# Kernel tuning notes

Hardware: AMD Instinct MI355X
Metric: run time of the kernel (lower is better)

The kernel has to match this reference:

```python
import jax, jax.numpy as jnp
import numpy as np

HID, NH, NKV, HD = 2048, 16, 8, 128
EPS = 1e-6
THETA = 10000.0
SCALE = HD ** -0.5


def setup_inputs() -> dict:
    key = jax.random.key(0)
    ks = jax.random.split(key, 6)
    S = 2048
    return {
        "positions": jnp.arange(S, dtype=jnp.int32),
        "hidden_states": jax.random.normal(ks[0], (S, HID), dtype=jnp.float32),
        "layernorm_weight": jax.random.uniform(ks[1], (HID,), dtype=jnp.float32, minval=0.5, maxval=1.5),
        "w_qkv": jax.random.normal(ks[2], ((NH + 2 * NKV) * HD, HID), dtype=jnp.float32) * 0.02,
        "w_o": jax.random.normal(ks[3], (HID, NH * HD), dtype=jnp.float32) * 0.02,
        "q_norm_w": jax.random.uniform(ks[4], (HD,), dtype=jnp.float32, minval=0.5, maxval=1.5),
        "k_norm_w": jax.random.uniform(ks[5], (HD,), dtype=jnp.float32, minval=0.5, maxval=1.5),
    }


def _rmsnorm(x, w, eps=EPS):
    var = jnp.mean(jnp.square(x), axis=-1, keepdims=True)
    return x * jax.lax.rsqrt(var + eps) * w


def _rope(x, cos, sin):
    # x: [S, h, HD]; cos/sin: [S, 1, HD//2] (neox-style rotate-half)
    x1, x2 = x[..., : HD // 2], x[..., HD // 2 :]
    return jnp.concatenate([x1 * cos - x2 * sin, x2 * cos + x1 * sin], axis=-1)


def reference(positions, hidden_states, layernorm_weight, w_qkv, w_o, q_norm_w, k_norm_w):
    S = hidden_states.shape[0]
    # Fused RMSNorm + QKV projection
    hn = _rmsnorm(hidden_states, layernorm_weight)
    qkv = hn @ w_qkv.T  # [S, (NH+2*NKV)*HD]
    q, k, v = jnp.split(qkv, [NH * HD, (NH + NKV) * HD], axis=-1)
    q = q.reshape(S, NH, HD)
    k = k.reshape(S, NKV, HD)
    v = v.reshape(S, NKV, HD)
    # Per-head QK RMSNorm
    q = _rmsnorm(q, q_norm_w)
    k = _rmsnorm(k, k_norm_w)
    # RoPE
    inv_freq = 1.0 / (THETA ** (jnp.arange(0, HD, 2, dtype=jnp.float32) / HD))
    freqs = positions.astype(jnp.float32)[:, None] * inv_freq  # [S, HD//2]
    cos = jnp.cos(freqs)[:, None, :]
    sin = jnp.sin(freqs)[:, None, :]
    q = _rope(q, cos, sin)
    k = _rope(k, cos, sin)
    # GQA: expand kv heads to match query heads
    rep = NH // NKV
    k = jnp.repeat(k, rep, axis=1)  # [S, NH, HD]
    v = jnp.repeat(v, rep, axis=1)
    # Causal attention
    scores = jnp.einsum("shd,thd->hst", q, k) * SCALE  # [NH, S, S]
    causal = jnp.tril(jnp.ones((S, S), dtype=bool))
    scores = jnp.where(causal, scores, jnp.finfo(scores.dtype).min)
    probs = jax.nn.softmax(scores, axis=-1)
    out = jnp.einsum("hst,thd->shd", probs, v)  # [S, NH, HD]
    # Output projection
    return out.reshape(S, NH * HD) @ w_o.T
```

## Files before the change

### kernel.cpp

```cpp
#include <hip/hip_runtime.h>
#include <hip/hip_bf16.h>
#include <math.h>

#define HID 2048
#define NH 16
#define NKV 8
#define HD 128
#define SEQ 2048
#define EPS 1e-6f
#define SCALE 0.08838834764831845f

typedef __attribute__((ext_vector_type(8))) short bf8_t;
typedef __attribute__((ext_vector_type(4))) float f4_t;

__device__ __forceinline__ short f2bf(float f) {
    union { __hip_bfloat16 h; short s; } u;
    u.h = __float2bfloat16(f);
    return u.s;
}
__device__ __forceinline__ float bf2f(short s) {
    union { short s; __hip_bfloat16 h; } u;
    u.s = s;
    return __bfloat162float(u.h);
}
__device__ __forceinline__ bf8_t pack8(const float4& a, const float4& b) {
    bf8_t r;
    r[0] = f2bf(a.x); r[1] = f2bf(a.y); r[2] = f2bf(a.z); r[3] = f2bf(a.w);
    r[4] = f2bf(b.x); r[5] = f2bf(b.y); r[6] = f2bf(b.z); r[7] = f2bf(b.w);
    return r;
}
__device__ __forceinline__ void gload16(const short* g, short* l) {
    __builtin_amdgcn_global_load_lds(
        (const __attribute__((address_space(1))) unsigned int*)g,
        (__attribute__((address_space(3))) unsigned int*)l, 16, 0, 0);
}

__device__ __forceinline__ float wave_reduce_sum(float v) {
#pragma unroll
    for (int off = 32; off > 0; off >>= 1) v += __shfl_xor(v, off);
    return v;
}

__global__ __launch_bounds__(256) void f2bf_kernel(
    const float* __restrict__ src, short* __restrict__ dst, int n8) {
    int i = blockIdx.x * 256 + threadIdx.x;
    if (i < n8) {
        float4 a = *(const float4*)(src + (size_t)i * 8);
        float4 b = *(const float4*)(src + (size_t)i * 8 + 4);
        *(bf8_t*)(dst + (size_t)i * 8) = pack8(a, b);
    }
}

__global__ __launch_bounds__(256) void rmsnorm_hid_kernel(
    const float* __restrict__ x, const float* __restrict__ w,
    short* __restrict__ out) {
    int row = blockIdx.x;
    int tid = threadIdx.x;
    const float* xr = x + (size_t)row * HID;
    float4 a = *(const float4*)(xr + tid * 8);
    float4 b = *(const float4*)(xr + tid * 8 + 4);
    float ss = a.x * a.x + a.y * a.y + a.z * a.z + a.w * a.w +
               b.x * b.x + b.y * b.y + b.z * b.z + b.w * b.w;
    ss = wave_reduce_sum(ss);
    __shared__ float part[4];
    __shared__ float s_scale;
    if ((tid & 63) == 0) part[tid >> 6] = ss;
    __syncthreads();
    if (tid == 0) {
        float t = part[0] + part[1] + part[2] + part[3];
        s_scale = rsqrtf(t / (float)HID + EPS);
    }
    __syncthreads();
    float sc = s_scale;
    float4 wa = *(const float4*)(w + tid * 8);
    float4 wb = *(const float4*)(w + tid * 8 + 4);
    float4 oa = make_float4(a.x * sc * wa.x, a.y * sc * wa.y,
                            a.z * sc * wa.z, a.w * sc * wa.w);
    float4 ob = make_float4(b.x * sc * wb.x, b.y * sc * wb.y,
                            b.z * sc * wb.z, b.w * sc * wb.w);
    *(bf8_t*)(out + (size_t)row * HID + tid * 8) = pack8(oa, ob);
}

template <int MODE>
__global__ __launch_bounds__(256) void gemm_mfma_kernel(
    const short* __restrict__ A, const short* __restrict__ B,
    float* __restrict__ Cf, short* __restrict__ Q, short* __restrict__ Kp,
    short* __restrict__ Vr, int M, int N, int K) {
    __shared__ short As[128][64];
    __shared__ short Bs[128][64];
    int tid = threadIdx.x;
    int wv = tid >> 6, lane = tid & 63;
    int n16 = lane & 15, qd = lane >> 4;
    int m0 = blockIdx.y * 128, n0 = blockIdx.x * 128;
    int wm = (wv >> 1) * 64, wn = (wv & 1) * 64;
    int sr8 = lane >> 3, slot = lane & 7;

    size_t ainv[4], binv[4];
#pragma unroll
    for (int it = 0; it < 4; ++it) {
        int row = wv * 32 + it * 8 + sr8;
        int chunk = (slot - row) & 7;
        ainv[it] = (size_t)(m0 + row) * K + chunk * 8;
        binv[it] = (size_t)(n0 + row) * K + chunk * 8;
    }

    f4_t acc[4][4];
#pragma unroll
    for (int i = 0; i < 4; ++i)
#pragma unroll
        for (int j = 0; j < 4; ++j) acc[i][j] = (f4_t){0.f, 0.f, 0.f, 0.f};

    for (int k0 = 0; k0 < K; k0 += 64) {
        __syncthreads();
#pragma unroll
        for (int it = 0; it < 4; ++it) {
            gload16(A + ainv[it] + k0, &As[wv * 32 + it * 8][0]);
            gload16(B + binv[it] + k0, &Bs[wv * 32 + it * 8][0]);
        }
        __syncthreads();

        bf8_t af[4][2], bf[4][2];
#pragma unroll
        for (int t = 0; t < 4; ++t)
#pragma unroll
            for (int ks = 0; ks < 2; ++ks) {
                int ar = wm + t * 16 + n16;
                af[t][ks] = *(const bf8_t*)&As[ar][(((ks * 4 + qd) + ar) & 7) * 8];
                int br = wn + t * 16 + n16;
                bf[t][ks] = *(const bf8_t*)&Bs[br][(((ks * 4 + qd) + br) & 7) * 8];
            }
#pragma unroll
        for (int ks = 0; ks < 2; ++ks)
#pragma unroll
            for (int mt = 0; mt < 4; ++mt)
#pragma unroll
                for (int nt = 0; nt < 4; ++nt)
                    acc[mt][nt] = __builtin_amdgcn_mfma_f32_16x16x32_bf16(
                        af[mt][ks], bf[nt][ks], acc[mt][nt], 0, 0, 0);
    }

#pragma unroll
    for (int mt = 0; mt < 4; ++mt)
#pragma unroll
        for (int nt = 0; nt < 4; ++nt)
#pragma unroll
            for (int r = 0; r < 4; ++r) {
                int gm = m0 + wm + mt * 16 + qd * 4 + r;
                int gn = n0 + wn + nt * 16 + n16;
                float v = acc[mt][nt][r];
                if (MODE == 0) {
                    Cf[(size_t)gm * N + gn] = v;
                } else {
                    if (gn < NH * HD)
                        Q[(size_t)gm * (NH * HD) + gn] = f2bf(v);
                    else if (gn < (NH + NKV) * HD)
                        Kp[(size_t)gm * (NKV * HD) + (gn - NH * HD)] = f2bf(v);
                    else
                        Vr[(size_t)gm * (NKV * HD) + (gn - (NH + NKV) * HD)] = f2bf(v);
                }
            }
}

__global__ __launch_bounds__(256) void transpose_v_kernel(
    const short* __restrict__ vr, short* __restrict__ vt) {
    __shared__ short t[64][64];
    int s0 = blockIdx.x * 64, d0 = blockIdx.y * 64;
    int tid = threadIdx.x;
    int sl = tid >> 3, ch = tid & 7;
#pragma unroll
    for (int it = 0; it < 2; ++it) {
        int s_local = it * 32 + sl;
        bf8_t vv = *(const bf8_t*)(vr + (size_t)(s0 + s_local) * (NKV * HD) + d0 + ch * 8);
        *(bf8_t*)&t[s_local][((ch + s_local) & 7) * 8] = vv;
    }
    __syncthreads();
#pragma unroll
    for (int it = 0; it < 2; ++it) {
        int d_local = it * 32 + sl;
        int sbase = ch * 8;
        bf8_t o;
#pragma unroll
        for (int j = 0; j < 8; ++j) {
            int s = sbase + j;
            o[j] = t[s][(((d_local >> 3) + s) & 7) * 8 + (d_local & 7)];
        }
        *(bf8_t*)(vt + (size_t)(d0 + d_local) * SEQ + s0 + sbase) = o;
    }
}

__global__ __launch_bounds__(128) void qknorm_rope_kernel(
    short* __restrict__ q, short* __restrict__ k,
    const float* __restrict__ qw, const float* __restrict__ kw,
    const int* __restrict__ pos) {
    int s = blockIdx.x;
    int hh = blockIdx.y;
    int d = threadIdx.x;
    short* ptr;
    const float* w;
    if (hh < NH) {
        ptr = q + (size_t)s * (NH * HD) + hh * HD;
        w = qw;
    } else {
        ptr = k + (size_t)s * (NKV * HD) + (hh - NH) * HD;
        w = kw;
    }
    float x = bf2f(ptr[d]);
    float ss = wave_reduce_sum(x * x);
    __shared__ float part[2];
    if ((d & 63) == 0) part[d >> 6] = ss;
    __syncthreads();
    float tot = part[0] + part[1];
    float xn = x * rsqrtf(tot / (float)HD + EPS) * w[d];
    __shared__ float sh[HD];
    sh[d] = xn;
    __syncthreads();
    int j = d & 63;
    float inv = powf(10000.0f, -(float)(2 * j) * (1.0f / (float)HD));
    float fr = (float)pos[s] * inv;
    float sn, cs;
    sincosf(fr, &sn, &cs);
    float o;
    if (d < 64)
        o = xn * cs - sh[d + 64] * sn;
    else
        o = xn * cs + sh[d - 64] * sn;
    ptr[d] = f2bf(o);
}

__device__ __forceinline__ void attn_stage(
    short (&kb)[64][128], short (&vb)[128][64],
    const short* __restrict__ kg, const short* __restrict__ vg,
    int t0, const int (&kinv)[4], const int (&vinv)[4], int wv) {
#pragma unroll
    for (int it = 0; it < 4; ++it) {
        gload16(kg + (size_t)t0 * (NKV * HD) + kinv[it], &kb[wv * 16 + it * 4][0]);
        gload16(vg + t0 + vinv[it], &vb[wv * 32 + it * 8][0]);
    }
}

__device__ __forceinline__ void attn_tile(
    const short (&kb)[64][128], const short (&vb)[128][64],
    short (&psh)[4][16][72],
    const bf8_t (&qf)[4], f4_t (&of)[8],
    float (&m_i)[4], float (&l_p)[4],
    int wv, int n, int qd, bool diag) {
    f4_t sc[4];
#pragma unroll
    for (int kk = 0; kk < 4; ++kk) sc[kk] = (f4_t){0.f, 0.f, 0.f, 0.f};
#pragma unroll
    for (int kk = 0; kk < 4; ++kk) {
        int key = kk * 16 + n;
#pragma unroll
        for (int ks = 0; ks < 4; ++ks) {
            bf8_t kf = *(const bf8_t*)&kb[key][(((ks * 4 + qd) + key) & 15) * 8];
            sc[kk] = __builtin_amdgcn_mfma_f32_16x16x32_bf16(qf[ks], kf, sc[kk], 0, 0, 0);
        }
    }
    int rowb = wv * 16 + qd * 4;
#pragma unroll
    for (int kk = 0; kk < 4; ++kk)
#pragma unroll
        for (int r = 0; r < 4; ++r) {
            float s = sc[kk][r] * SCALE;
            if (diag && (kk * 16 + n > rowb + r)) s = -1e30f;
            sc[kk][r] = s;
        }
#pragma unroll
    for (int r = 0; r < 4; ++r) {
        float mx = fmaxf(fmaxf(sc[0][r], sc[1][r]), fmaxf(sc[2][r], sc[3][r]));
#pragma unroll
        for (int off = 1; off < 16; off <<= 1) mx = fmaxf(mx, __shfl_xor(mx, off));
        float mnew = fmaxf(m_i[r], mx);
        float al = __expf(m_i[r] - mnew);
        m_i[r] = mnew;
        float lsum = 0.f;
#pragma unroll
        for (int kk = 0; kk < 4; ++kk) {
            float p = __expf(sc[kk][r] - mnew);
            psh[wv][qd * 4 + r][kk * 16 + n] = f2bf(p);
            lsum += p;
        }
        l_p[r] = l_p[r] * al + lsum;
#pragma unroll
        for (int nb = 0; nb < 8; ++nb) of[nb][r] *= al;
    }
    __builtin_amdgcn_wave_barrier();
#pragma unroll
    for (int ks2 = 0; ks2 < 2; ++ks2) {
        bf8_t pf = *(const bf8_t*)&psh[wv][n][ks2 * 32 + qd * 8];
#pragma unroll
        for (int nb = 0; nb < 8; ++nb) {
            int dim = nb * 16 + n;
            bf8_t vf = *(const bf8_t*)&vb[dim][(((ks2 * 4 + qd) + dim) & 7) * 8];
            of[nb] = __builtin_amdgcn_mfma_f32_16x16x32_bf16(pf, vf, of[nb], 0, 0, 0);
        }
    }
}

__global__ __launch_bounds__(256) void attn_mfma_kernel(
    const short* __restrict__ q, const short* __restrict__ k,
    const short* __restrict__ vt, short* __restrict__ o) {
    __shared__ short kbufA[64][128], kbufB[64][128];
    __shared__ short vbufA[128][64], vbufB[128][64];
    __shared__ short psh[4][16][72];

    int tid = threadIdx.x;
    int wv = tid >> 6, lane = tid & 63;
    int n = lane & 15, qd = lane >> 4;
    int bid = blockIdx.x;
    int p = bid & 255;
    int h, qb;
    if (bid < 256) { h = p >> 5;       qb = 31 - (p & 31); }
    else           { h = 8 + (p >> 5); qb = p & 31; }
    int kvh = h >> 1;
    int qbase = qb * 64;

    int kinv[4], vinv[4];
#pragma unroll
    for (int it = 0; it < 4; ++it) {
        int key = wv * 16 + it * 4 + (lane >> 4);
        int ck = ((lane & 15) - key) & 15;
        kinv[it] = key * (NKV * HD) + kvh * HD + ck * 8;
        int dim = wv * 32 + it * 8 + (lane >> 3);
        int cv = ((lane & 7) - dim) & 7;
        vinv[it] = (kvh * HD + dim) * SEQ + cv * 8;
    }

    bf8_t qf[4];
    {
        const short* qp = q + (size_t)(qbase + wv * 16 + n) * (NH * HD) + h * HD + qd * 8;
#pragma unroll
        for (int ks = 0; ks < 4; ++ks) qf[ks] = *(const bf8_t*)(qp + ks * 32);
    }

    f4_t of[8];
#pragma unroll
    for (int i = 0; i < 8; ++i) of[i] = (f4_t){0.f, 0.f, 0.f, 0.f};
    float m_i[4] = {-1e30f, -1e30f, -1e30f, -1e30f};
    float l_p[4] = {0.f, 0.f, 0.f, 0.f};

    int ntiles = qb + 1;
    attn_stage(kbufA, vbufA, k, vt, 0, kinv, vinv, wv);
    for (int tt = 0; tt < ntiles; tt += 2) {
        __syncthreads();
        if (tt + 1 < ntiles)
            attn_stage(kbufB, vbufB, k, vt, (tt + 1) * 64, kinv, vinv, wv);
        attn_tile(kbufA, vbufA, psh, qf, of, m_i, l_p, wv, n, qd, tt == qb);
        if (tt + 1 < ntiles) {
            __syncthreads();
            if (tt + 2 < ntiles)
                attn_stage(kbufA, vbufA, k, vt, (tt + 2) * 64, kinv, vinv, wv);
            attn_tile(kbufB, vbufB, psh, qf, of, m_i, l_p, wv, n, qd, tt + 1 == qb);
        }
    }

    float inv[4];
#pragma unroll
    for (int r = 0; r < 4; ++r) {
        float l = l_p[r];
#pragma unroll
        for (int off = 1; off < 16; off <<= 1) l += __shfl_xor(l, off);
        inv[r] = 1.0f / l;
    }
#pragma unroll
    for (int nb = 0; nb < 8; ++nb)
#pragma unroll
        for (int r = 0; r < 4; ++r) {
            int row = qbase + wv * 16 + qd * 4 + r;
            o[(size_t)row * (NH * HD) + h * HD + nb * 16 + n] = f2bf(of[nb][r] * inv[r]);
        }
}

extern "C" void kernel_launch(void* const* d_in, const int* in_sizes, int n_in,
                              void* d_out, int out_size, void* d_ws, size_t ws_size,
                              hipStream_t stream) {
    const int* positions   = (const int*)d_in[0];
    const float* hidden    = (const float*)d_in[1];
    const float* ln_w      = (const float*)d_in[2];
    const float* w_qkv     = (const float*)d_in[3];
    const float* w_o       = (const float*)d_in[4];
    const float* q_norm_w  = (const float*)d_in[5];
    const float* k_norm_w  = (const float*)d_in[6];
    float* out = (float*)d_out;

    char* base = (char*)d_ws;
    short* hnb  = (short*)(base);
    short* wqb  = (short*)(base + ((size_t)8 << 20));
    short* vtb  = (short*)(base + ((size_t)8 << 20));
    short* wob  = (short*)(base + ((size_t)24 << 20));
    short* qbf  = (short*)(base + ((size_t)32 << 20));
    short* kbf  = (short*)(base + ((size_t)40 << 20));
    short* vrow = (short*)(base + ((size_t)44 << 20));

    f2bf_kernel<<<4096, 256, 0, stream>>>(w_qkv, wqb, (NH + 2 * NKV) * HD * HID / 8);
    f2bf_kernel<<<2048, 256, 0, stream>>>(w_o, wob, HID * NH * HD / 8);
    rmsnorm_hid_kernel<<<SEQ, 256, 0, stream>>>(hidden, ln_w, hnb);
    gemm_mfma_kernel<1><<<dim3(32, 16), 256, 0, stream>>>(
        hnb, wqb, nullptr, qbf, kbf, vrow, SEQ, (NH + 2 * NKV) * HD, HID);
    transpose_v_kernel<<<dim3(SEQ / 64, NKV * HD / 64), 256, 0, stream>>>(vrow, vtb);
    qknorm_rope_kernel<<<dim3(SEQ, NH + NKV), 128, 0, stream>>>(
        qbf, kbf, q_norm_w, k_norm_w, positions);
    attn_mfma_kernel<<<512, 256, 0, stream>>>(qbf, kbf, vtb, hnb);
    gemm_mfma_kernel<0><<<dim3(16, 16), 256, 0, stream>>>(
        hnb, wob, out, nullptr, nullptr, nullptr, SEQ, NH * HD, HID);
}
```

Baseline: 293.0 us.

## Split long causal attention rows into KV chunks with merge; fuse small prep kernels

Attention for the upper 16 query blocks is split into two KV chunks, each computed by its own workgroup that writes unnormalised bf16 partials plus running max and sum. A new merge kernel combines the two chunks with log-sum-exp weights. This balances work across 768 workgroups instead of 512 uneven ones. The weight conversions and hidden-state RMSNorm are fused into one launch, as are the V transpose and QK-norm/RoPE, to cut launch count. The cost is an extra kernel, partial-result traffic, and bf16 rounding of the partials before the merge.

```diff
diff --git a/kernel.cpp b/kernel.cpp
--- a/kernel.cpp
+++ b/kernel.cpp
@@ -41,21 +41,28 @@
     return v;
 }
 
-__global__ __launch_bounds__(256) void f2bf_kernel(
-    const float* __restrict__ src, short* __restrict__ dst, int n8) {
-    int i = blockIdx.x * 256 + threadIdx.x;
-    if (i < n8) {
-        float4 a = *(const float4*)(src + (size_t)i * 8);
-        float4 b = *(const float4*)(src + (size_t)i * 8 + 4);
-        *(bf8_t*)(dst + (size_t)i * 8) = pack8(a, b);
-    }
-}
-
-__global__ __launch_bounds__(256) void rmsnorm_hid_kernel(
+__global__ __launch_bounds__(256) void prep_kernel(
+    const float* __restrict__ w_qkv, short* __restrict__ wqb,
+    const float* __restrict__ w_o, short* __restrict__ wob,
     const float* __restrict__ x, const float* __restrict__ w,
     short* __restrict__ out) {
-    int row = blockIdx.x;
+    int bid = blockIdx.x;
     int tid = threadIdx.x;
+    if (bid < 4096) {
+        int i = bid * 256 + tid;
+        float4 a = *(const float4*)(w_qkv + (size_t)i * 8);
+        float4 b = *(const float4*)(w_qkv + (size_t)i * 8 + 4);
+        *(bf8_t*)(wqb + (size_t)i * 8) = pack8(a, b);
+        return;
+    }
+    if (bid < 6144) {
+        int i = (bid - 4096) * 256 + tid;
+        float4 a = *(const float4*)(w_o + (size_t)i * 8);
+        float4 b = *(const float4*)(w_o + (size_t)i * 8 + 4);
+        *(bf8_t*)(wob + (size_t)i * 8) = pack8(a, b);
+        return;
+    }
+    int row = bid - 6144;
     const float* xr = x + (size_t)row * HID;
     float4 a = *(const float4*)(xr + tid * 8);
     float4 b = *(const float4*)(xr + tid * 8 + 4);
@@ -161,40 +168,41 @@
             }
 }
 
-__global__ __launch_bounds__(256) void transpose_v_kernel(
-    const short* __restrict__ vr, short* __restrict__ vt) {
-    __shared__ short t[64][64];
-    int s0 = blockIdx.x * 64, d0 = blockIdx.y * 64;
-    int tid = threadIdx.x;
-    int sl = tid >> 3, ch = tid & 7;
-#pragma unroll
-    for (int it = 0; it < 2; ++it) {
-        int s_local = it * 32 + sl;
-        bf8_t vv = *(const bf8_t*)(vr + (size_t)(s0 + s_local) * (NKV * HD) + d0 + ch * 8);
-        *(bf8_t*)&t[s_local][((ch + s_local) & 7) * 8] = vv;
-    }
-    __syncthreads();
-#pragma unroll
-    for (int it = 0; it < 2; ++it) {
-        int d_local = it * 32 + sl;
-        int sbase = ch * 8;
-        bf8_t o;
-#pragma unroll
-        for (int j = 0; j < 8; ++j) {
-            int s = sbase + j;
-            o[j] = t[s][(((d_local >> 3) + s) & 7) * 8 + (d_local & 7)];
-        }
-        *(bf8_t*)(vt + (size_t)(d0 + d_local) * SEQ + s0 + sbase) = o;
-    }
-}
-
-__global__ __launch_bounds__(128) void qknorm_rope_kernel(
+__global__ __launch_bounds__(256) void mid_kernel(
+    const short* __restrict__ vr, short* __restrict__ vt,
     short* __restrict__ q, short* __restrict__ k,
     const float* __restrict__ qw, const float* __restrict__ kw,
     const int* __restrict__ pos) {
-    int s = blockIdx.x;
-    int hh = blockIdx.y;
-    int d = threadIdx.x;
+    int bid = blockIdx.x;
+    int tid = threadIdx.x;
+    if (bid < 512) {
+        __shared__ short t[64][64];
+        int s0 = (bid & 31) * 64, d0 = (bid >> 5) * 64;
+        int sl = tid >> 3, ch = tid & 7;
+#pragma unroll
+        for (int it = 0; it < 2; ++it) {
+            int s_local = it * 32 + sl;
+            bf8_t vv = *(const bf8_t*)(vr + (size_t)(s0 + s_local) * (NKV * HD) + d0 + ch * 8);
+            *(bf8_t*)&t[s_local][((ch + s_local) & 7) * 8] = vv;
+        }
+        __syncthreads();
+#pragma unroll
+        for (int it = 0; it < 2; ++it) {
+            int d_local = it * 32 + sl;
+            int sbase = ch * 8;
+            bf8_t o;
+#pragma unroll
+            for (int j = 0; j < 8; ++j) {
+                int s = sbase + j;
+                o[j] = t[s][(((d_local >> 3) + s) & 7) * 8 + (d_local & 7)];
+            }
+            *(bf8_t*)(vt + (size_t)(d0 + d_local) * SEQ + s0 + sbase) = o;
+        }
+        return;
+    }
+    int u = (bid - 512) * 2 + (tid >> 7);
+    int ui = tid >> 7, d = tid & 127;
+    int s = u / 24, hh = u % 24;
     short* ptr;
     const float* w;
     if (hh < NH) {
@@ -206,13 +214,13 @@
     }
     float x = bf2f(ptr[d]);
     float ss = wave_reduce_sum(x * x);
-    __shared__ float part[2];
-    if ((d & 63) == 0) part[d >> 6] = ss;
+    __shared__ float part[2][2];
+    if ((d & 63) == 0) part[ui][d >> 6] = ss;
     __syncthreads();
-    float tot = part[0] + part[1];
+    float tot = part[ui][0] + part[ui][1];
     float xn = x * rsqrtf(tot / (float)HD + EPS) * w[d];
-    __shared__ float sh[HD];
-    sh[d] = xn;
+    __shared__ float sh[2][HD];
+    sh[ui][d] = xn;
     __syncthreads();
     int j = d & 63;
     float inv = powf(10000.0f, -(float)(2 * j) * (1.0f / (float)HD));
@@ -221,9 +229,9 @@
     sincosf(fr, &sn, &cs);
     float o;
     if (d < 64)
-        o = xn * cs - sh[d + 64] * sn;
+        o = xn * cs - sh[ui][d + 64] * sn;
     else
-        o = xn * cs + sh[d - 64] * sn;
+        o = xn * cs + sh[ui][d - 64] * sn;
     ptr[d] = f2bf(o);
 }
 
@@ -297,9 +305,10 @@
     }
 }
 
-__global__ __launch_bounds__(256) void attn_mfma_kernel(
+__global__ __launch_bounds__(256) void attn_chunk_kernel(
     const short* __restrict__ q, const short* __restrict__ k,
-    const short* __restrict__ vt, short* __restrict__ o) {
+    const short* __restrict__ vt, short* __restrict__ o,
+    short* __restrict__ opart, float* __restrict__ ml) {
     __shared__ short kbufA[64][128], kbufB[64][128];
     __shared__ short vbufA[128][64], vbufB[128][64];
     __shared__ short psh[4][16][72];
@@ -307,11 +316,26 @@
     int tid = threadIdx.x;
     int wv = tid >> 6, lane = tid & 63;
     int n = lane & 15, qd = lane >> 4;
+
     int bid = blockIdx.x;
-    int p = bid & 255;
-    int h, qb;
-    if (bid < 256) { h = p >> 5;       qb = 31 - (p & 31); }
-    else           { h = 8 + (p >> 5); qb = p & 31; }
+    int h, qb, tstart, tcount, c;
+    bool split;
+    if (bid < 512) {
+        int id = bid;
+        qb = 16 + (id >> 5);
+        c = (id >> 4) & 1;
+        h = id & 15;
+        if (c == 0) { tstart = 0; tcount = 16; }
+        else        { tstart = 16; tcount = qb - 15; }
+        split = true;
+    } else {
+        int id = bid - 512;
+        qb = 15 - (id >> 4);
+        h = id & 15;
+        tstart = 0; tcount = qb + 1; c = 0;
+        split = false;
+    }
+    bool dl = (tstart + tcount - 1 == qb);
     int kvh = h >> 1;
     int qbase = qb * 64;
 
@@ -339,36 +363,85 @@
     float m_i[4] = {-1e30f, -1e30f, -1e30f, -1e30f};
     float l_p[4] = {0.f, 0.f, 0.f, 0.f};
 
-    int ntiles = qb + 1;
-    attn_stage(kbufA, vbufA, k, vt, 0, kinv, vinv, wv);
-    for (int tt = 0; tt < ntiles; tt += 2) {
+    attn_stage(kbufA, vbufA, k, vt, tstart * 64, kinv, vinv, wv);
+    for (int tt = 0; tt < tcount; tt += 2) {
         __syncthreads();
-        if (tt + 1 < ntiles)
-            attn_stage(kbufB, vbufB, k, vt, (tt + 1) * 64, kinv, vinv, wv);
-        attn_tile(kbufA, vbufA, psh, qf, of, m_i, l_p, wv, n, qd, tt == qb);
-        if (tt + 1 < ntiles) {
+        if (tt + 1 < tcount)
+            attn_stage(kbufB, vbufB, k, vt, (tstart + tt + 1) * 64, kinv, vinv, wv);
+        attn_tile(kbufA, vbufA, psh, qf, of, m_i, l_p, wv, n, qd, dl && (tt == tcount - 1));
+        if (tt + 1 < tcount) {
             __syncthreads();
-            if (tt + 2 < ntiles)
-                attn_stage(kbufA, vbufA, k, vt, (tt + 2) * 64, kinv, vinv, wv);
-            attn_tile(kbufB, vbufB, psh, qf, of, m_i, l_p, wv, n, qd, tt + 1 == qb);
-        }
-    }
-
-    float inv[4];
+            if (tt + 2 < tcount)
+                attn_stage(kbufA, vbufA, k, vt, (tstart + tt + 2) * 64, kinv, vinv, wv);
+            attn_tile(kbufB, vbufB, psh, qf, of, m_i, l_p, wv, n, qd, dl && (tt + 1 == tcount - 1));
+        }
+    }
+
+    float lred[4];
 #pragma unroll
     for (int r = 0; r < 4; ++r) {
         float l = l_p[r];
 #pragma unroll
         for (int off = 1; off < 16; off <<= 1) l += __shfl_xor(l, off);
-        inv[r] = 1.0f / l;
-    }
-#pragma unroll
-    for (int nb = 0; nb < 8; ++nb)
-#pragma unroll
-        for (int r = 0; r < 4; ++r) {
-            int row = qbase + wv * 16 + qd * 4 + r;
-            o[(size_t)row * (NH * HD) + h * HD + nb * 16 + n] = f2bf(of[nb][r] * inv[r]);
-        }
+        lred[r] = l;
+    }
+
+    if (!split) {
+#pragma unroll
+        for (int nb = 0; nb < 8; ++nb)
+#pragma unroll
+            for (int r = 0; r < 4; ++r) {
+                int row = qbase + wv * 16 + qd * 4 + r;
+                o[(size_t)row * (NH * HD) + h * HD + nb * 16 + n] =
+                    f2bf(of[nb][r] / lred[r]);
+            }
+    } else {
+        size_t pb = ((size_t)h * 16 + (qb - 16)) * 2 + c;
+        short* op = opart + pb * (64 * 128);
+#pragma unroll
+        for (int nb = 0; nb < 8; ++nb)
+#pragma unroll
+            for (int r = 0; r < 4; ++r) {
+                int rl = wv * 16 + qd * 4 + r;
+                op[rl * 128 + nb * 16 + n] = f2bf(of[nb][r]);
+            }
+        if (n == 0) {
+#pragma unroll
+            for (int r = 0; r < 4; ++r) {
+                int rl = wv * 16 + qd * 4 + r;
+                ml[pb * 128 + rl * 2] = m_i[r];
+                ml[pb * 128 + rl * 2 + 1] = lred[r];
+            }
+        }
+    }
+}
+
+__global__ __launch_bounds__(256) void attn_merge_kernel(
+    const short* __restrict__ opart, const float* __restrict__ ml,
+    short* __restrict__ o) {
+    int bid = blockIdx.x;
+    int h = bid & 15, qi = bid >> 4;
+    int tid = threadIdx.x;
+    int r = tid >> 2, dq = tid & 3;
+    size_t pb0 = ((size_t)h * 16 + qi) * 2;
+    size_t pb1 = pb0 + 1;
+    float m0 = ml[pb0 * 128 + r * 2], l0 = ml[pb0 * 128 + r * 2 + 1];
+    float m1 = ml[pb1 * 128 + r * 2], l1 = ml[pb1 * 128 + r * 2 + 1];
+    float M = fmaxf(m0, m1);
+    float w0 = __expf(m0 - M), w1 = __expf(m1 - M);
+    float invL = 1.0f / (w0 * l0 + w1 * l1);
+    int row = (16 + qi) * 64 + r;
+#pragma unroll
+    for (int j = 0; j < 4; ++j) {
+        int d0 = dq * 32 + j * 8;
+        bf8_t a = *(const bf8_t*)(opart + pb0 * (64 * 128) + r * 128 + d0);
+        bf8_t b = *(const bf8_t*)(opart + pb1 * (64 * 128) + r * 128 + d0);
+        bf8_t e;
+#pragma unroll
+        for (int i = 0; i < 8; ++i)
+            e[i] = f2bf((w0 * bf2f(a[i]) + w1 * bf2f(b[i])) * invL);
+        *(bf8_t*)(o + (size_t)row * (NH * HD) + h * HD + d0) = e;
+    }
 }
 
 extern "C" void kernel_launch(void* const* d_in, const int* in_sizes, int n_in,
@@ -384,23 +457,23 @@
     float* out = (float*)d_out;
 
     char* base = (char*)d_ws;
-    short* hnb  = (short*)(base);
-    short* wqb  = (short*)(base + ((size_t)8 << 20));
-    short* vtb  = (short*)(base + ((size_t)8 << 20));
-    short* wob  = (short*)(base + ((size_t)24 << 20));
-    short* qbf  = (short*)(base + ((size_t)32 << 20));
-    short* kbf  = (short*)(base + ((size_t)40 << 20));
-    short* vrow = (short*)(base + ((size_t)44 << 20));
-
-    f2bf_kernel<<<4096, 256, 0, stream>>>(w_qkv, wqb, (NH + 2 * NKV) * HD * HID / 8);
-    f2bf_kernel<<<2048, 256, 0, stream>>>(w_o, wob, HID * NH * HD / 8);
-    rmsnorm_hid_kernel<<<SEQ, 256, 0, stream>>>(hidden, ln_w, hnb);
+    short* hnb   = (short*)(base);
+    short* wqb   = (short*)(base + ((size_t)8 << 20));
+    short* vtb   = (short*)(base + ((size_t)8 << 20));
+    short* opart = (short*)(base + ((size_t)12 << 20));
+    float* mlbuf = (float*)(base + ((size_t)20 << 20));
+    short* wob   = (short*)(base + ((size_t)24 << 20));
+    short* qbf   = (short*)(base + ((size_t)32 << 20));
+    short* kbf   = (short*)(base + ((size_t)40 << 20));
+    short* vrow  = (short*)(base + ((size_t)44 << 20));
+
+    prep_kernel<<<8192, 256, 0, stream>>>(w_qkv, wqb, w_o, wob, hidden, ln_w, hnb);
     gemm_mfma_kernel<1><<<dim3(32, 16), 256, 0, stream>>>(
         hnb, wqb, nullptr, qbf, kbf, vrow, SEQ, (NH + 2 * NKV) * HD, HID);
-    transpose_v_kernel<<<dim3(SEQ / 64, NKV * HD / 64), 256, 0, stream>>>(vrow, vtb);
-    qknorm_rope_kernel<<<dim3(SEQ, NH + NKV), 128, 0, stream>>>(
-        qbf, kbf, q_norm_w, k_norm_w, positions);
-    attn_mfma_kernel<<<512, 256, 0, stream>>>(qbf, kbf, vtb, hnb);
+    mid_kernel<<<512 + 24576, 256, 0, stream>>>(
+        vrow, vtb, qbf, kbf, q_norm_w, k_norm_w, positions);
+    attn_chunk_kernel<<<768, 256, 0, stream>>>(qbf, kbf, vtb, hnb, opart, mlbuf);
+    attn_merge_kernel<<<256, 256, 0, stream>>>(opart, mlbuf, hnb);
     gemm_mfma_kernel<0><<<dim3(16, 16), 256, 0, stream>>>(
         hnb, wob, out, nullptr, nullptr, nullptr, SEQ, NH * HD, HID);
 }
```

Result: slower. 300.8 us (+2.6%).
